# Kernel tuning notes

Measured on AMD Instinct MI355X. Metric: run time of the kernel, lower is better.

Reference implementation:

```python
import jax, jax.numpy as jnp
import numpy as np
from jax import lax

WIN = (1, 1, 2, 2, 2)  # MaxPool3d(2)/AvgPool3d(2): kernel=stride=2 over (H,W,D)


def _maxpool3d(v):
    return lax.reduce_window(v, -jnp.inf, lax.max, WIN, WIN, 'VALID')


def _avgpool3d(v):
    s = lax.reduce_window(v, 0.0, lax.add, WIN, WIN, 'VALID')
    return s / 8.0  # 2*2*2 window


def setup_inputs() -> dict:
    key = jax.random.key(0)
    kx, ky, kz = jax.random.split(key, 3)
    shape = (4, 256, 32, 32, 32)
    return {
        'x': jax.random.normal(kx, shape, dtype=jnp.float32),
        'y': jax.random.normal(ky, shape, dtype=jnp.float32),
        'z': jax.random.normal(kz, shape, dtype=jnp.float32),
    }


def reference(x, y, z):
    b, c = x.shape[0], x.shape[1]
    # pool + add (max + avg), then flatten spatial dims
    xp = (_maxpool3d(x) + _avgpool3d(x)).reshape(b, c, -1)
    yp = (_maxpool3d(y) + _avgpool3d(y)).reshape(b, c, -1)
    zp = (_maxpool3d(z) + _avgpool3d(z)).reshape(b, c, -1)
    # einsum('bci,bcj->bcij', v, v).sum over (i,j) == (sum_i v_i)^2 per (b,c);
    # compute the algebraically identical reduced form to avoid the b*c*n^2 tensor.
    s_xy = jnp.sum(xp + yp, axis=2)
    s_xz = jnp.sum(xp + zp, axis=2)
    s_yz = jnp.sum(yp + zp, axis=2)
    pooled = s_xy * s_xy + s_yz * s_yz + s_xz * s_xz  # [b, c]
    # F.normalize(pooled, dim=-1): L2 normalize with eps=1e-12
    norm = jnp.linalg.norm(pooled, axis=-1, keepdims=True)
    return pooled / jnp.maximum(norm, 1e-12)
```

## Files before the change

kernel.cpp:

```cpp
#include <hip/hip_runtime.h>
#include <math.h>


#define BC_TOTAL 1024
#define SLICE_ELEMS 32768

__global__ __launch_bounds__(256) void pool_sum_kernel(
    const float* __restrict__ x,
    const float* __restrict__ y,
    const float* __restrict__ z,
    float* __restrict__ ws)
{
    const int bc = blockIdx.x;
    const int which = blockIdx.y;
    const float* __restrict__ p =
        (which == 0 ? x : (which == 1 ? y : z)) + (size_t)bc * SLICE_ELEMS;

    const int t = threadIdx.x;
    const float* __restrict__ q =
        p + ((t >> 7) * 2048 + ((t >> 3) & 15) * 64 + (t & 7) * 4);

    float acc0 = 0.0f, acc1 = 0.0f;

#pragma unroll
    for (int g = 0; g < 2; ++g) {
        float4 v[16];
#pragma unroll
        for (int j = 0; j < 4; ++j) {
            const float* __restrict__ r = q + (g * 4 + j) * 4096;
            v[4 * j + 0] = *reinterpret_cast<const float4*>(r);
            v[4 * j + 1] = *reinterpret_cast<const float4*>(r + 32);
            v[4 * j + 2] = *reinterpret_cast<const float4*>(r + 1024);
            v[4 * j + 3] = *reinterpret_cast<const float4*>(r + 1056);
        }
#pragma unroll
        for (int j = 0; j < 4; ++j) {
            const float4 a0 = v[4 * j + 0];
            const float4 a1 = v[4 * j + 1];
            const float4 a2 = v[4 * j + 2];
            const float4 a3 = v[4 * j + 3];

            const float mx = fmaxf(fmaxf(a0.x, a1.x), fmaxf(a2.x, a3.x));
            const float my = fmaxf(fmaxf(a0.y, a1.y), fmaxf(a2.y, a3.y));
            const float mz = fmaxf(fmaxf(a0.z, a1.z), fmaxf(a2.z, a3.z));
            const float mw = fmaxf(fmaxf(a0.w, a1.w), fmaxf(a2.w, a3.w));

            const float s = ((a0.x + a0.y) + (a0.z + a0.w))
                          + ((a1.x + a1.y) + (a1.z + a1.w))
                          + ((a2.x + a2.y) + (a2.z + a2.w))
                          + ((a3.x + a3.y) + (a3.z + a3.w));

            const float contrib = fmaxf(mx, my) + fmaxf(mz, mw) + s * 0.125f;
            if (j & 1) acc1 += contrib; else acc0 += contrib;
        }
    }

    float acc = acc0 + acc1;

#pragma unroll
    for (int off = 32; off > 0; off >>= 1) acc += __shfl_down(acc, off);

    __shared__ float red[4];
    const int wave = t >> 6;
    if ((t & 63) == 0) red[wave] = acc;
    __syncthreads();
    if (t == 0) {
        ws[which * BC_TOTAL + bc] = (red[0] + red[1]) + (red[2] + red[3]);
    }
}

__global__ __launch_bounds__(256) void finalize_kernel(
    const float* __restrict__ ws, float* __restrict__ out)
{
    const int b = blockIdx.x;
    const int c = threadIdx.x;
    const int bc = b * 256 + c;

    const float Sx = ws[bc];
    const float Sy = ws[BC_TOTAL + bc];
    const float Sz = ws[2 * BC_TOTAL + bc];

    const float xy = Sx + Sy;
    const float yz = Sy + Sz;
    const float xz = Sx + Sz;
    const float pooled = xy * xy + yz * yz + xz * xz;

    float sq = pooled * pooled;
#pragma unroll
    for (int off = 32; off > 0; off >>= 1) sq += __shfl_down(sq, off);

    __shared__ float red[4];
    if ((c & 63) == 0) red[c >> 6] = sq;
    __syncthreads();

    __shared__ float norm_s;
    if (c == 0) norm_s = sqrtf((red[0] + red[1]) + (red[2] + red[3]));
    __syncthreads();

    const float norm = fmaxf(norm_s, 1e-12f);
    out[bc] = pooled / norm;
}

extern "C" void kernel_launch(void* const* d_in, const int* in_sizes, int n_in,
                              void* d_out, int out_size, void* d_ws, size_t ws_size,
                              hipStream_t stream) {
    const float* x = (const float*)d_in[0];
    const float* y = (const float*)d_in[1];
    const float* z = (const float*)d_in[2];
    float* ws = (float*)d_ws;
    float* out = (float*)d_out;

    dim3 grid(BC_TOTAL, 3, 1);
    pool_sum_kernel<<<grid, 256, 0, stream>>>(x, y, z, ws);
    finalize_kernel<<<4, 256, 0, stream>>>(ws, out);
}
```

Measured before the change: 74.72 us.

## Merge x/y/z into one 512-thread block per slice

Replaces the 3D grid of 256-thread blocks (one per tensor per slice) with one 512-thread block per (b,c) slice that processes x, y and z in sequence and reduces all three sums together. Each thread now issues 16 float4 loads per tensor, with a sched_barrier placed after the loads so they are issued before any compute. The aim is fewer blocks and less per-block reduction and launch overhead, with more loads in flight per thread. The cost is fewer total waves in the grid and higher register pressure from the unrolled three-tensor loop.

```diff
diff --git a/kernel.cpp b/kernel.cpp
--- a/kernel.cpp
+++ b/kernel.cpp
@@ -5,40 +5,42 @@
 #define BC_TOTAL 1024
 #define SLICE_ELEMS 32768
 
-__global__ __launch_bounds__(256) void pool_sum_kernel(
+__global__ __launch_bounds__(512) void pool_sum_kernel(
     const float* __restrict__ x,
     const float* __restrict__ y,
     const float* __restrict__ z,
     float* __restrict__ ws)
 {
     const int bc = blockIdx.x;
-    const int which = blockIdx.y;
-    const float* __restrict__ p =
-        (which == 0 ? x : (which == 1 ? y : z)) + (size_t)bc * SLICE_ELEMS;
+    const int t = threadIdx.x;
 
-    const int t = threadIdx.x;
-    const float* __restrict__ q =
-        p + ((t >> 7) * 2048 + ((t >> 3) & 15) * 64 + (t & 7) * 4);
+    const int off0 = (t >> 7) * 2048 + ((t >> 3) & 15) * 64 + (t & 7) * 4;
 
-    float acc0 = 0.0f, acc1 = 0.0f;
+    float acc[3];
 
 #pragma unroll
-    for (int g = 0; g < 2; ++g) {
+    for (int w = 0; w < 3; ++w) {
+        const float* __restrict__ q =
+            (w == 0 ? x : (w == 1 ? y : z)) + (size_t)bc * SLICE_ELEMS + off0;
+
         float4 v[16];
 #pragma unroll
-        for (int j = 0; j < 4; ++j) {
-            const float* __restrict__ r = q + (g * 4 + j) * 4096;
-            v[4 * j + 0] = *reinterpret_cast<const float4*>(r);
-            v[4 * j + 1] = *reinterpret_cast<const float4*>(r + 32);
-            v[4 * j + 2] = *reinterpret_cast<const float4*>(r + 1024);
-            v[4 * j + 3] = *reinterpret_cast<const float4*>(r + 1056);
+        for (int it = 0; it < 4; ++it) {
+            const float* __restrict__ r = q + it * 8192;
+            v[4 * it + 0] = *reinterpret_cast<const float4*>(r);
+            v[4 * it + 1] = *reinterpret_cast<const float4*>(r + 32);
+            v[4 * it + 2] = *reinterpret_cast<const float4*>(r + 1024);
+            v[4 * it + 3] = *reinterpret_cast<const float4*>(r + 1056);
         }
+        __builtin_amdgcn_sched_barrier(0);
+
+        float a0s = 0.0f, a1s = 0.0f;
 #pragma unroll
-        for (int j = 0; j < 4; ++j) {
-            const float4 a0 = v[4 * j + 0];
-            const float4 a1 = v[4 * j + 1];
-            const float4 a2 = v[4 * j + 2];
-            const float4 a3 = v[4 * j + 3];
+        for (int it = 0; it < 4; ++it) {
+            const float4 a0 = v[4 * it + 0];
+            const float4 a1 = v[4 * it + 1];
+            const float4 a2 = v[4 * it + 2];
+            const float4 a3 = v[4 * it + 3];
 
             const float mx = fmaxf(fmaxf(a0.x, a1.x), fmaxf(a2.x, a3.x));
             const float my = fmaxf(fmaxf(a0.y, a1.y), fmaxf(a2.y, a3.y));
@@ -51,21 +53,31 @@
                           + ((a3.x + a3.y) + (a3.z + a3.w));
 
             const float contrib = fmaxf(mx, my) + fmaxf(mz, mw) + s * 0.125f;
-            if (j & 1) acc1 += contrib; else acc0 += contrib;
+            if (it & 1) a1s += contrib; else a0s += contrib;
         }
+        acc[w] = a0s + a1s;
     }
 
-    float acc = acc0 + acc1;
+#pragma unroll
+    for (int off = 32; off > 0; off >>= 1) {
+        acc[0] += __shfl_down(acc[0], off);
+        acc[1] += __shfl_down(acc[1], off);
+        acc[2] += __shfl_down(acc[2], off);
+    }
 
+    __shared__ float red[8][3];
+    const int wave = t >> 6;
+    if ((t & 63) == 0) {
+        red[wave][0] = acc[0];
+        red[wave][1] = acc[1];
+        red[wave][2] = acc[2];
+    }
+    __syncthreads();
+    if (t < 3) {
+        float s = 0.0f;
 #pragma unroll
-    for (int off = 32; off > 0; off >>= 1) acc += __shfl_down(acc, off);
-
-    __shared__ float red[4];
-    const int wave = t >> 6;
-    if ((t & 63) == 0) red[wave] = acc;
-    __syncthreads();
-    if (t == 0) {
-        ws[which * BC_TOTAL + bc] = (red[0] + red[1]) + (red[2] + red[3]);
+        for (int wv = 0; wv < 8; ++wv) s += red[wv][t];
+        ws[t * BC_TOTAL + bc] = s;
     }
 }
 
@@ -110,7 +122,6 @@
     float* ws = (float*)d_ws;
     float* out = (float*)d_out;
 
-    dim3 grid(BC_TOTAL, 3, 1);
-    pool_sum_kernel<<<grid, 256, 0, stream>>>(x, y, z, ws);
+    pool_sum_kernel<<<BC_TOTAL, 512, 0, stream>>>(x, y, z, ws);
     finalize_kernel<<<4, 256, 0, stream>>>(ws, out);
 }
```

Result: no change. 74.18 us, median of 2 (-0.7%).
